# Optimization experiments

Measured on AMD Instinct MI355X. Metric: run time of the kernel, lower is better.

## Reference

```python
import jax, jax.numpy as jnp
import numpy as np

H = 128      # hidden_size
L = 2        # num_layers
IN0 = 96     # seq_feature_size + context_feature_size
OUT = 1

def _xavier(k, shape):
    fan_out, fan_in = shape
    lim = (6.0 / (fan_in + fan_out)) ** 0.5
    return jax.random.uniform(k, shape, jnp.float32, -lim, lim)

def _orth(k, n):
    q, _ = jnp.linalg.qr(jax.random.normal(k, (n, n)))
    return q.astype(jnp.float32)

def setup_inputs() -> dict:
    key = jax.random.key(0)
    ks = jax.random.split(key, 16)
    B, S, F_seq, F_ctx = 512, 512, 64, 32
    inp = {
        "seq_features": jax.random.normal(ks[0], (B, S, F_seq), jnp.float32),
        "context_features": jax.random.normal(ks[1], (B, F_ctx), jnp.float32),
    }
    for i in range(L):
        in_size = IN0 if i == 0 else H
        inp[f"tau{i}"] = jax.random.normal(ks[2 + 5 * i], (H,), jnp.float32) * 0.1
        inp[f"Win{i}"] = _xavier(ks[3 + 5 * i], (H, in_size))
        inp[f"Wrec{i}"] = _orth(ks[4 + 5 * i], H)
        inp[f"Wg{i}"] = _xavier(ks[5 + 5 * i], (H, in_size + H))
        inp[f"bg{i}"] = jnp.zeros((H,), jnp.float32)
    inp["W1"] = _xavier(ks[12], (H // 2, H))
    inp["b1"] = jnp.zeros((H // 2,), jnp.float32)
    inp["W2"] = _xavier(ks[13], (OUT, H // 2))
    inp["b2"] = jnp.zeros((OUT,), jnp.float32)
    return inp

def _cell_step(x, h, tau_p, Win, Wrec, Wg, bg):
    # LTC cell: RK4 integration of dh/dt = -h/tau + W_in x + gate * W_rec h
    tau = jax.nn.softplus(tau_p) + 1.0
    def rhs(hh):
        gate = jax.nn.sigmoid(jnp.tanh(jnp.concatenate([x, hh], axis=-1) @ Wg.T + bg))
        return -hh / tau + x @ Win.T + gate * (hh @ Wrec.T)
    k1 = rhs(h)
    k2 = rhs(h + 0.5 * k1)
    k3 = rhs(h + 0.5 * k2)
    k4 = rhs(h + k3)
    return jnp.tanh(h + (k1 + 2.0 * k2 + 2.0 * k3 + k4) / 6.0)

def reference(seq_features, context_features, tau0, Win0, Wrec0, Wg0, bg0,
              tau1, Win1, Wrec1, Wg1, bg1, W1, b1, W2, b2):
    B, S, _ = seq_features.shape
    ctx = jnp.broadcast_to(context_features[:, None, :], (B, S, context_features.shape[-1]))
    x = jnp.concatenate([seq_features, ctx], axis=-1)     # [B,S,IN0]
    xs = jnp.swapaxes(x, 0, 1)                            # [S,B,IN0] time-major
    cells = [(tau0, Win0, Wrec0, Wg0, bg0), (tau1, Win1, Wrec1, Wg1, bg1)]
    h_init = tuple(jnp.zeros((B, H), x.dtype) for _ in range(L))

    def step(hs, xt):
        new = []
        inp = xt
        for hi, p in zip(hs, cells):
            hn = _cell_step(inp, hi, *p)
            new.append(hn)
            inp = hn
        return tuple(new), None

    hs, _ = jax.lax.scan(step, h_init, xs)
    h_last = hs[-1]                                       # [B,H]
    # classifier (dropout is identity in eval mode)
    out = jax.nn.sigmoid(jax.nn.relu(h_last @ W1.T + b1) @ W2.T + b2)
    return out.reshape(B, -1)
```

## Files before the change

### kernel.cpp

```cpp
#include <hip/hip_runtime.h>


typedef _Float16 f16;
typedef _Float16 f16x4 __attribute__((ext_vector_type(4)));
typedef _Float16 f16x8 __attribute__((ext_vector_type(8)));
typedef float f32x4 __attribute__((ext_vector_type(4)));

#define NSTEP 512
#define OFF_A0 0
#define OFF_A1 32768
#define OFF_AIO 65536
#define OFF_AX 98304
#define W_TOTAL 122880

#define HQ0 0
#define HQ1 4352
#define L0A 8704
#define L0B 13056
#define L1A 17408
#define L1B 21760
#define L1H 26112
#define XT0 30464
#define XT1 32768
#define SMEM_BYTES 35072

__device__ __forceinline__ float rcp_f(float x) { return __builtin_amdgcn_rcpf(x); }
__device__ __forceinline__ float tanh_f(float x) {
  float e = __expf(2.f * x);
  return 1.f - 2.f * rcp_f(e + 1.f);
}
__device__ __forceinline__ float sig_poly(float t) {
  float s = t * t;
  float p = fmaf(s, 2.1356861e-5f, -2.1081349e-4f);
  p = fmaf(s, p, 2.0833333e-3f);
  p = fmaf(s, p, -2.0833333e-2f);
  p = fmaf(s, p, 0.25f);
  return fmaf(t, p, 0.5f);
}

#define BAR()                                            \
  do {                                                   \
    asm volatile("s_waitcnt lgkmcnt(0)" ::: "memory");   \
    __builtin_amdgcn_s_barrier();                        \
  } while (0)

__global__ __launch_bounds__(256) void prep_kernel(
    const float* __restrict__ Win0, const float* __restrict__ Wrec0,
    const float* __restrict__ Wg0, const float* __restrict__ Win1,
    const float* __restrict__ Wrec1, const float* __restrict__ Wg1,
    f16* __restrict__ W) {
  int i = blockIdx.x * 256 + threadIdx.x;
  if (i >= W_TOTAL) return;
  if (i < OFF_AX) {
    int sec = i >> 15;
    int r = i & 32767;
    int j = r & 7, lane = (r >> 3) & 63, kc = (r >> 9) & 3, sel = (r >> 11) & 1,
        w = (r >> 12) & 7;
    int row = w * 16 + (lane & 15);
    int k = kc * 32 + ((lane >> 4) << 3) + j;
    float v;
    if (sec == 0)
      v = sel ? Wrec0[row * 128 + k] : Wg0[row * 224 + 96 + k];
    else if (sec == 1)
      v = sel ? Wrec1[row * 128 + k] : Wg1[row * 256 + 128 + k];
    else
      v = sel ? Wg1[row * 256 + k] : Win1[row * 128 + k];
    W[i] = (f16)v;
  } else {
    int r = i - OFF_AX;
    int j = r & 7, lane = (r >> 3) & 63, g = r >> 9;
    int kc = g % 3, sg = g / 3;
    int sel = sg & 1, w = sg >> 1;
    int row = w * 16 + (lane & 15);
    int k = kc * 32 + ((lane >> 4) << 3) + j;
    W[i] = (f16)(sel ? Wg0[row * 224 + k] : Win0[row * 96 + k]);
  }
}

#define MFMA16(A, B, C) __builtin_amdgcn_mfma_f32_16x16x32_f16((A), (B), (C), 0, 0, 0)
#define ZERO4 ((f32x4){0.f, 0.f, 0.f, 0.f})

#define MM2(SRC)                                                    \
  {                                                                 \
    const f16* bp_ = (SRC) + c * 136 + 8 * q;                       \
    _Pragma("unroll") for (int kc_ = 0; kc_ < 4; ++kc_) {           \
      f16x8 bf_ = *(const f16x8*)(bp_ + kc_ * 32);                  \
      ga[0] = MFMA16(awg[0][kc_], bf_, ga[0]);                      \
      ra[0] = MFMA16(awr[0][kc_], bf_, ra[0]);                      \
      ga[1] = MFMA16(awg[1][kc_], bf_, ga[1]);                      \
      ra[1] = MFMA16(awr[1][kc_], bf_, ra[1]);                      \
    }                                                               \
  }

#define MMIO(SRC, KCN)                                              \
  {                                                                 \
    const f16* bp_ = (SRC) + c * 136 + 8 * q;                       \
    _Pragma("unroll") for (int kc_ = 0; kc_ < (KCN); ++kc_) {       \
      f16x8 bf_ = *(const f16x8*)(bp_ + kc_ * 32);                  \
      ga[0] = MFMA16(au[0][kc_], bf_, ga[0]);                       \
      ra[0] = MFMA16(ag2[0][kc_], bf_, ra[0]);                      \
      ga[1] = MFMA16(au[1][kc_], bf_, ga[1]);                       \
      ra[1] = MFMA16(ag2[1][kc_], bf_, ra[1]);                      \
    }                                                               \
  }

#define XPROJ(XSRC, UD, GD)                                         \
  {                                                                 \
    ZACC;                                                           \
    f16x8 bx0_ = *(const f16x8*)((XSRC) + c * 72 + 8 * q);          \
    f16x8 bx1_ = *(const f16x8*)((XSRC) + c * 72 + 32 + 8 * q);     \
    _Pragma("unroll") for (int i2_ = 0; i2_ < 2; ++i2_) {           \
      ga[i2_] = MFMA16(au[i2_][0], bx0_, ga[i2_]);                  \
      ra[i2_] = MFMA16(ag2[i2_][0], bx0_, ra[i2_]);                 \
      ga[i2_] = MFMA16(au[i2_][1], bx1_, ga[i2_]);                  \
      ra[i2_] = MFMA16(ag2[i2_][1], bx1_, ra[i2_]);                 \
      ga[i2_] = MFMA16(au[i2_][2], bctx, ga[i2_]);                  \
      ra[i2_] = MFMA16(ag2[i2_][2], bctx, ra[i2_]);                 \
      (UD)[i2_] = ga[i2_];                                          \
      _Pragma("unroll") for (int r_ = 0; r_ < 4; ++r_)              \
        (GD)[i2_][r_] = ra[i2_][r_] + bgv[i2_][r_];                 \
    }                                                               \
  }

#define GATEALL(WC, HC, DST)                                        \
  _Pragma("unroll") for (int i2_ = 0; i2_ < 2; ++i2_) {             \
    f16x4 hv_;                                                      \
    _Pragma("unroll") for (int r_ = 0; r_ < 4; ++r_) {              \
      float th_ = tanh_f(ga[i2_][r_] + gx[i2_][r_]);                \
      float gt_ = sig_poly(th_);                                    \
      float kk_ = fmaf(gt_, ra[i2_][r_],                            \
                       fmaf(-itv[i2_][r_], hhc[i2_][r_], u[i2_][r_])); \
      ksum[i2_][r_] = fmaf((WC), kk_, ksum[i2_][r_]);               \
      float hn_ = fmaf((HC), kk_, hst[i2_][r_]);                    \
      hhc[i2_][r_] = hn_;                                           \
      hv_[r_] = (f16)hn_;                                           \
    }                                                               \
    *(f16x4*)((DST) + c * 136 + jb[i2_]) = hv_;                     \
  }

#define GATEFIN(DST)                                                \
  _Pragma("unroll") for (int i2_ = 0; i2_ < 2; ++i2_) {             \
    f16x4 hv_;                                                      \
    _Pragma("unroll") for (int r_ = 0; r_ < 4; ++r_) {              \
      float th_ = tanh_f(ga[i2_][r_] + gx[i2_][r_]);                \
      float gt_ = sig_poly(th_);                                    \
      float kk_ = fmaf(gt_, ra[i2_][r_],                            \
                       fmaf(-itv[i2_][r_], hhc[i2_][r_], u[i2_][r_])); \
      float ks_ = ksum[i2_][r_] + kk_;                              \
      float hn_ = tanh_f(fmaf(ks_, 0.16666667f, hst[i2_][r_]));     \
      hst[i2_][r_] = hn_;                                           \
      hhc[i2_][r_] = hn_;                                           \
      hv_[r_] = (f16)hn_;                                           \
    }                                                               \
    *(f16x4*)((DST) + c * 136 + jb[i2_]) = hv_;                     \
  }

#define ZACC { ga[0] = ZERO4; ra[0] = ZERO4; ga[1] = ZERO4; ra[1] = ZERO4; }

__global__ __launch_bounds__(512, 1) void ltc_kernel(
    const float* __restrict__ seq, const float* __restrict__ ctx,
    const float* __restrict__ tau0p, const float* __restrict__ bg0p,
    const float* __restrict__ tau1p, const float* __restrict__ bg1p,
    const float* __restrict__ W1, const float* __restrict__ b1,
    const float* __restrict__ W2, const float* __restrict__ b2,
    const f16* __restrict__ W, float* __restrict__ out) {
  __shared__ __align__(16) char smem[SMEM_BYTES];
  f16* hq0 = (f16*)(smem + HQ0);
  f16* hq1 = (f16*)(smem + HQ1);
  f16* l0a = (f16*)(smem + L0A);
  f16* l0b = (f16*)(smem + L0B);
  f16* l1a = (f16*)(smem + L1A);
  f16* l1b = (f16*)(smem + L1B);
  f16* l1h = (f16*)(smem + L1H);
  f16* xt0 = (f16*)(smem + XT0);
  f16* xt1 = (f16*)(smem + XT1);

  const int tid = threadIdx.x;
  const int w8 = tid >> 6, lane = tid & 63;
  const int q = lane >> 4, c = lane & 15;
  const int wl = w8 & 3;
  const bool isL0 = (w8 < 4);
  const int bg = blockIdx.x;
  int jb[2];
  jb[0] = 32 * wl + 4 * q;
  jb[1] = jb[0] + 16;

  f16* bufA = isL0 ? l0a : l1a;
  f16* bufB = isL0 ? l0b : l1b;

  f16x8 awg[2][4], awr[2][4], au[2][4], ag2[2][4];
  f16x8 bctx;
  if (isL0) {
#pragma unroll
    for (int i2 = 0; i2 < 2; ++i2) {
      int T = 2 * wl + i2;
#pragma unroll
      for (int kc = 0; kc < 4; ++kc) {
        awg[i2][kc] = *(const f16x8*)(W + OFF_A0 + (((T * 2 + 0) * 4 + kc) * 64 + lane) * 8);
        awr[i2][kc] = *(const f16x8*)(W + OFF_A0 + (((T * 2 + 1) * 4 + kc) * 64 + lane) * 8);
      }
#pragma unroll
      for (int kc = 0; kc < 3; ++kc) {
        au[i2][kc] = *(const f16x8*)(W + OFF_AX + (((T * 2 + 0) * 3 + kc) * 64 + lane) * 8);
        ag2[i2][kc] = *(const f16x8*)(W + OFF_AX + (((T * 2 + 1) * 3 + kc) * 64 + lane) * 8);
      }
      au[i2][3] = (f16x8)(f16)0.f;
      ag2[i2][3] = (f16x8)(f16)0.f;
    }
    const float* cp = ctx + (bg * 16 + c) * 32 + 8 * q;
#pragma unroll
    for (int j = 0; j < 8; ++j) bctx[j] = (f16)cp[j];
  } else {
#pragma unroll
    for (int i2 = 0; i2 < 2; ++i2) {
      int T = 2 * wl + i2;
#pragma unroll
      for (int kc = 0; kc < 4; ++kc) {
        awg[i2][kc] = *(const f16x8*)(W + OFF_A1 + (((T * 2 + 0) * 4 + kc) * 64 + lane) * 8);
        awr[i2][kc] = *(const f16x8*)(W + OFF_A1 + (((T * 2 + 1) * 4 + kc) * 64 + lane) * 8);
        au[i2][kc] = *(const f16x8*)(W + OFF_AIO + (((T * 2 + 0) * 4 + kc) * 64 + lane) * 8);
        ag2[i2][kc] = *(const f16x8*)(W + OFF_AIO + (((T * 2 + 1) * 4 + kc) * 64 + lane) * 8);
      }
    }
  }

  const float* taup = isL0 ? tau0p : tau1p;
  const float* bgp = isL0 ? bg0p : bg1p;
  f32x4 itv[2], bgv[2];
#pragma unroll
  for (int i2 = 0; i2 < 2; ++i2)
#pragma unroll
    for (int r = 0; r < 4; ++r) {
      float t = taup[jb[i2] + r];
      itv[i2][r] = 1.f / (logf(1.f + __expf(t)) + 1.f);
      bgv[i2][r] = bgp[jb[i2] + r];
    }

  f32x4 hst[2], hhc[2], u[2], gx[2], ksum[2], ga[2], ra[2];
  f32x4 un[2], gxn[2];
  hst[0] = hst[1] = hhc[0] = hhc[1] = ZERO4;
  ksum[0] = ksum[1] = ZERO4;
  un[0] = un[1] = gxn[0] = gxn[1] = ZERO4;

  for (int j = tid; j < 2176; j += 512) {
    hq1[j] = (f16)0.f;
    l1h[j] = (f16)0.f;
  }
  const int bs = tid >> 4, fp = tid & 15;
  const size_t seqrow = ((size_t)(bg * 16 + bs)) * NSTEP * 64 + 4 * fp;
  float4 sq_nxt = {0.f, 0.f, 0.f, 0.f};
  float4 sq_ld = sq_nxt;
  if (tid < 256) {
    float4 sv = *(const float4*)(seq + seqrow);
    *(f16x4*)(xt0 + bs * 72 + 4 * fp) =
        (f16x4){(f16)sv.x, (f16)sv.y, (f16)sv.z, (f16)sv.w};
    sq_nxt = *(const float4*)(seq + seqrow + 64);
  }
  __syncthreads();
  if (isL0) { XPROJ(xt0, u, gx); }

#pragma unroll 1
  for (int i = 0; i <= NSTEP; ++i) {
    const f16* hprev = ((i + 1) & 1) ? hq1 : hq0;
    f16* xw = ((i + 1) & 1) ? xt1 : xt0;

    if (isL0) {
      if (i < NSTEP) {
        if (i + 2 < NSTEP)
          sq_ld = *(const float4*)(seq + seqrow + (size_t)(i + 2) * 64);
        ZACC;
        MM2(hprev);
        if (i + 1 < NSTEP)
          *(f16x4*)(xw + bs * 72 + 4 * fp) =
              (f16x4){(f16)sq_nxt.x, (f16)sq_nxt.y, (f16)sq_nxt.z, (f16)sq_nxt.w};
        ksum[0] = ZERO4; ksum[1] = ZERO4;
        GATEALL(1.0f, 0.5f, bufA);
      }
    } else {
      if (i >= 1) {
        ZACC;
        MMIO(hprev, 4);
#pragma unroll
        for (int i2 = 0; i2 < 2; ++i2) {
          u[i2] = ga[i2];
#pragma unroll
          for (int r = 0; r < 4; ++r) gx[i2][r] = ra[i2][r] + bgv[i2][r];
        }
        ZACC;
        MM2(l1h);
        ksum[0] = ZERO4; ksum[1] = ZERO4;
        GATEALL(1.0f, 0.5f, bufA);
      }
    }
    BAR();

    if (isL0) {
      if (i < NSTEP) {
        ZACC;
        MM2(bufA);
        GATEALL(2.0f, 0.5f, bufB);
        if (i + 1 < NSTEP) { XPROJ(xw, un, gxn); }
      }
    } else if (i >= 1) {
      ZACC;
      MM2(bufA);
      GATEALL(2.0f, 0.5f, bufB);
    }
    BAR();

    if ((isL0 && i < NSTEP) || (!isL0 && i >= 1)) {
      ZACC;
      MM2(bufB);
      GATEALL(2.0f, 1.0f, bufA);
    }
    BAR();

    if (isL0) {
      if (i < NSTEP) {
        ZACC;
        MM2(bufA);
        GATEFIN((i & 1) ? hq1 : hq0);
        if (i + 1 < NSTEP) {
          u[0] = un[0]; u[1] = un[1];
          gx[0] = gxn[0]; gx[1] = gxn[1];
          if (i + 2 < NSTEP) sq_nxt = sq_ld;
        }
      }
    } else if (i >= 1) {
      ZACC;
      MM2(bufA);
      GATEFIN(l1h);
    }
    BAR();
  }

  float* h1f = (float*)smem;
  if (!isL0) {
#pragma unroll
    for (int i2 = 0; i2 < 2; ++i2)
      *(f32x4*)(h1f + c * 132 + jb[i2]) = hst[i2];
  }
  __syncthreads();
  float* z1 = (float*)(smem + 16 * 132 * 4);
  {
    int b = tid >> 5, o = tid & 31;
#pragma unroll
    for (int hlf = 0; hlf < 2; ++hlf) {
      int oo = o + 32 * hlf;
      const float* wr = W1 + oo * 128;
      const float* hr = h1f + b * 132;
      float s = 0.f;
#pragma unroll
      for (int j = 0; j < 128; j += 4) {
        f32x4 wv = *(const f32x4*)(wr + j);
        f32x4 hv = *(const f32x4*)(hr + j);
        s += wv[0] * hv[0] + wv[1] * hv[1] + wv[2] * hv[2] + wv[3] * hv[3];
      }
      s += b1[oo];
      z1[b * 64 + oo] = fmaxf(s, 0.f);
    }
  }
  __syncthreads();
  if (tid < 16) {
    float s = b2[0];
#pragma unroll
    for (int o = 0; o < 64; ++o) s += z1[tid * 64 + o] * W2[o];
    out[bg * 16 + tid] = rcp_f(1.f + __expf(-s));
  }
}

extern "C" void kernel_launch(void* const* d_in, const int* in_sizes, int n_in,
                              void* d_out, int out_size, void* d_ws, size_t ws_size,
                              hipStream_t stream) {
  (void)in_sizes; (void)n_in; (void)out_size; (void)ws_size;
  const float* seq = (const float*)d_in[0];
  const float* ctx = (const float*)d_in[1];
  const float* tau0 = (const float*)d_in[2];
  const float* Win0 = (const float*)d_in[3];
  const float* Wrec0 = (const float*)d_in[4];
  const float* Wg0 = (const float*)d_in[5];
  const float* bg0 = (const float*)d_in[6];
  const float* tau1 = (const float*)d_in[7];
  const float* Win1 = (const float*)d_in[8];
  const float* Wrec1 = (const float*)d_in[9];
  const float* Wg1 = (const float*)d_in[10];
  const float* bg1 = (const float*)d_in[11];
  const float* W1 = (const float*)d_in[12];
  const float* b1 = (const float*)d_in[13];
  const float* W2 = (const float*)d_in[14];
  const float* b2 = (const float*)d_in[15];
  f16* W = (f16*)d_ws;

  prep_kernel<<<480, 256, 0, stream>>>(Win0, Wrec0, Wg0, Win1, Wrec1, Wg1, W);
  ltc_kernel<<<32, 512, 0, stream>>>(seq, ctx, tau0, bg0, tau1, bg1, W1, b1, W2,
                                     b2, W, (float*)d_out);
}
```

Before: 1.922 ms.

## Split LTC layers across producer and consumer blocks with global ring buffer

Layer 0 and layer 1 now run in separate workgroups (64 blocks total) instead of splitting one 512-thread block into two 4-wave halves. Layer 0 producer blocks push each timestep's hidden state through a 4-slot global ring, guarded by acquire/release flags, to layer 1 consumer blocks. Each wave now owns one 16-row tile instead of two, which halves per-wave MFMA and gate work on the serial critical path and uses more CUs. The cost is cross-CU spin-wait synchronisation through L2 every step, which adds latency and depends on all 64 blocks being co-resident.

```diff
diff --git a/kernel.cpp b/kernel.cpp
--- a/kernel.cpp
+++ b/kernel.cpp
@@ -5,6 +5,7 @@
 typedef _Float16 f16x4 __attribute__((ext_vector_type(4)));
 typedef _Float16 f16x8 __attribute__((ext_vector_type(8)));
 typedef float f32x4 __attribute__((ext_vector_type(4)));
+typedef unsigned long long u64;
 
 #define NSTEP 512
 #define OFF_A0 0
@@ -13,16 +14,18 @@
 #define OFF_AX 98304
 #define W_TOTAL 122880
 
+#define FLAGS_OFF 245760
+#define RING_OFF 246272
+#define RING_R 4
+#define RING_PAIR_BYTES (RING_R * 4096)
+
 #define HQ0 0
 #define HQ1 4352
-#define L0A 8704
-#define L0B 13056
-#define L1A 17408
-#define L1B 21760
-#define L1H 26112
-#define XT0 30464
-#define XT1 32768
-#define SMEM_BYTES 35072
+#define LBA 8704
+#define LBB 13056
+#define XT0 17408
+#define XT1 19712
+#define SMEM_BYTES 22272
 
 __device__ __forceinline__ float rcp_f(float x) { return __builtin_amdgcn_rcpf(x); }
 __device__ __forceinline__ float tanh_f(float x) {
@@ -49,6 +52,8 @@
     const float* __restrict__ Wg0, const float* __restrict__ Win1,
     const float* __restrict__ Wrec1, const float* __restrict__ Wg1,
     f16* __restrict__ W) {
+  if (blockIdx.x == 0 && threadIdx.x < 64)
+    ((int*)((char*)W + FLAGS_OFF))[threadIdx.x] = 0;
   int i = blockIdx.x * 256 + threadIdx.x;
   if (i >= W_TOTAL) return;
   if (i < OFF_AX) {
@@ -80,82 +85,68 @@
 #define MFMA16(A, B, C) __builtin_amdgcn_mfma_f32_16x16x32_f16((A), (B), (C), 0, 0, 0)
 #define ZERO4 ((f32x4){0.f, 0.f, 0.f, 0.f})
 
-#define MM2(SRC)                                                    \
-  {                                                                 \
+#define MM2G(SRC)                                                   \
+  {                                                                 \
+    ga = gx; ra = ZERO4;                                            \
     const f16* bp_ = (SRC) + c * 136 + 8 * q;                       \
     _Pragma("unroll") for (int kc_ = 0; kc_ < 4; ++kc_) {           \
       f16x8 bf_ = *(const f16x8*)(bp_ + kc_ * 32);                  \
-      ga[0] = MFMA16(awg[0][kc_], bf_, ga[0]);                      \
-      ra[0] = MFMA16(awr[0][kc_], bf_, ra[0]);                      \
-      ga[1] = MFMA16(awg[1][kc_], bf_, ga[1]);                      \
-      ra[1] = MFMA16(awr[1][kc_], bf_, ra[1]);                      \
+      ga = MFMA16(awg[kc_], bf_, ga);                               \
+      ra = MFMA16(awr[kc_], bf_, ra);                               \
     }                                                               \
   }
 
-#define MMIO(SRC, KCN)                                              \
-  {                                                                 \
-    const f16* bp_ = (SRC) + c * 136 + 8 * q;                       \
-    _Pragma("unroll") for (int kc_ = 0; kc_ < (KCN); ++kc_) {       \
-      f16x8 bf_ = *(const f16x8*)(bp_ + kc_ * 32);                  \
-      ga[0] = MFMA16(au[0][kc_], bf_, ga[0]);                       \
-      ra[0] = MFMA16(ag2[0][kc_], bf_, ra[0]);                      \
-      ga[1] = MFMA16(au[1][kc_], bf_, ga[1]);                       \
-      ra[1] = MFMA16(ag2[1][kc_], bf_, ra[1]);                      \
-    }                                                               \
+#define MMIO_PF()                                                   \
+  {                                                                 \
+    ga = ZERO4; ra = bgv;                                           \
+    ga = MFMA16(au[0], pf0, ga); ra = MFMA16(ag2[0], pf0, ra);      \
+    ga = MFMA16(au[1], pf1, ga); ra = MFMA16(ag2[1], pf1, ra);      \
+    ga = MFMA16(au[2], pf2, ga); ra = MFMA16(ag2[2], pf2, ra);      \
+    ga = MFMA16(au[3], pf3, ga); ra = MFMA16(ag2[3], pf3, ra);      \
+    u = ga; gx = ra;                                                \
   }
 
 #define XPROJ(XSRC, UD, GD)                                         \
   {                                                                 \
-    ZACC;                                                           \
+    f32x4 tg_ = ZERO4, tr_ = bgv;                                   \
     f16x8 bx0_ = *(const f16x8*)((XSRC) + c * 72 + 8 * q);          \
     f16x8 bx1_ = *(const f16x8*)((XSRC) + c * 72 + 32 + 8 * q);     \
-    _Pragma("unroll") for (int i2_ = 0; i2_ < 2; ++i2_) {           \
-      ga[i2_] = MFMA16(au[i2_][0], bx0_, ga[i2_]);                  \
-      ra[i2_] = MFMA16(ag2[i2_][0], bx0_, ra[i2_]);                 \
-      ga[i2_] = MFMA16(au[i2_][1], bx1_, ga[i2_]);                  \
-      ra[i2_] = MFMA16(ag2[i2_][1], bx1_, ra[i2_]);                 \
-      ga[i2_] = MFMA16(au[i2_][2], bctx, ga[i2_]);                  \
-      ra[i2_] = MFMA16(ag2[i2_][2], bctx, ra[i2_]);                 \
-      (UD)[i2_] = ga[i2_];                                          \
-      _Pragma("unroll") for (int r_ = 0; r_ < 4; ++r_)              \
-        (GD)[i2_][r_] = ra[i2_][r_] + bgv[i2_][r_];                 \
-    }                                                               \
+    tg_ = MFMA16(au[0], bx0_, tg_); tr_ = MFMA16(ag2[0], bx0_, tr_);\
+    tg_ = MFMA16(au[1], bx1_, tg_); tr_ = MFMA16(ag2[1], bx1_, tr_);\
+    tg_ = MFMA16(au[2], bctx, tg_); tr_ = MFMA16(ag2[2], bctx, tr_);\
+    (UD) = tg_; (GD) = tr_;                                         \
   }
 
 #define GATEALL(WC, HC, DST)                                        \
-  _Pragma("unroll") for (int i2_ = 0; i2_ < 2; ++i2_) {             \
+  {                                                                 \
     f16x4 hv_;                                                      \
     _Pragma("unroll") for (int r_ = 0; r_ < 4; ++r_) {              \
-      float th_ = tanh_f(ga[i2_][r_] + gx[i2_][r_]);                \
+      float th_ = tanh_f(ga[r_]);                                   \
       float gt_ = sig_poly(th_);                                    \
-      float kk_ = fmaf(gt_, ra[i2_][r_],                            \
-                       fmaf(-itv[i2_][r_], hhc[i2_][r_], u[i2_][r_])); \
-      ksum[i2_][r_] = fmaf((WC), kk_, ksum[i2_][r_]);               \
-      float hn_ = fmaf((HC), kk_, hst[i2_][r_]);                    \
-      hhc[i2_][r_] = hn_;                                           \
+      float kk_ = fmaf(gt_, ra[r_],                                 \
+                       fmaf(-itv[r_], hhc[r_], u[r_]));             \
+      ksum[r_] = fmaf((WC), kk_, ksum[r_]);                         \
+      float hn_ = fmaf((HC), kk_, hst[r_]);                         \
+      hhc[r_] = hn_;                                                \
       hv_[r_] = (f16)hn_;                                           \
     }                                                               \
-    *(f16x4*)((DST) + c * 136 + jb[i2_]) = hv_;                     \
-  }
-
-#define GATEFIN(DST)                                                \
-  _Pragma("unroll") for (int i2_ = 0; i2_ < 2; ++i2_) {             \
-    f16x4 hv_;                                                      \
-    _Pragma("unroll") for (int r_ = 0; r_ < 4; ++r_) {              \
-      float th_ = tanh_f(ga[i2_][r_] + gx[i2_][r_]);                \
-      float gt_ = sig_poly(th_);                                    \
-      float kk_ = fmaf(gt_, ra[i2_][r_],                            \
-                       fmaf(-itv[i2_][r_], hhc[i2_][r_], u[i2_][r_])); \
-      float ks_ = ksum[i2_][r_] + kk_;                              \
-      float hn_ = tanh_f(fmaf(ks_, 0.16666667f, hst[i2_][r_]));     \
-      hst[i2_][r_] = hn_;                                           \
-      hhc[i2_][r_] = hn_;                                           \
-      hv_[r_] = (f16)hn_;                                           \
-    }                                                               \
-    *(f16x4*)((DST) + c * 136 + jb[i2_]) = hv_;                     \
-  }
-
-#define ZACC { ga[0] = ZERO4; ra[0] = ZERO4; ga[1] = ZERO4; ra[1] = ZERO4; }
+    *(f16x4*)((DST) + c * 136 + jbase) = hv_;                       \
+  }
+
+#define LDPF8(KC_, DST_)                                                      \
+  {                                                                           \
+    u64* p_ = (u64*)(rs_ + c * 128 + (KC_) * 32 + 8 * q);                     \
+    u64 lo_ = __hip_atomic_load(p_, __ATOMIC_RELAXED, __HIP_MEMORY_SCOPE_AGENT); \
+    u64 hi_ = __hip_atomic_load(p_ + 1, __ATOMIC_RELAXED, __HIP_MEMORY_SCOPE_AGENT); \
+    union { u64 v[2]; f16x8 f; } uu_;                                         \
+    uu_.v[0] = lo_; uu_.v[1] = hi_;                                           \
+    DST_ = uu_.f;                                                             \
+  }
+#define LOADPF(M_)                                                  \
+  {                                                                 \
+    f16* rs_ = ring + ((M_) & (RING_R - 1)) * 2048;                 \
+    LDPF8(0, pf0); LDPF8(1, pf1); LDPF8(2, pf2); LDPF8(3, pf3);     \
+  }
 
 __global__ __launch_bounds__(512, 1) void ltc_kernel(
     const float* __restrict__ seq, const float* __restrict__ ctx,
@@ -163,183 +154,193 @@
     const float* __restrict__ tau1p, const float* __restrict__ bg1p,
     const float* __restrict__ W1, const float* __restrict__ b1,
     const float* __restrict__ W2, const float* __restrict__ b2,
-    const f16* __restrict__ W, float* __restrict__ out) {
+    const f16* __restrict__ W, char* __restrict__ ws,
+    float* __restrict__ out) {
   __shared__ __align__(16) char smem[SMEM_BYTES];
   f16* hq0 = (f16*)(smem + HQ0);
   f16* hq1 = (f16*)(smem + HQ1);
-  f16* l0a = (f16*)(smem + L0A);
-  f16* l0b = (f16*)(smem + L0B);
-  f16* l1a = (f16*)(smem + L1A);
-  f16* l1b = (f16*)(smem + L1B);
-  f16* l1h = (f16*)(smem + L1H);
+  f16* bufA = (f16*)(smem + LBA);
+  f16* bufB = (f16*)(smem + LBB);
   f16* xt0 = (f16*)(smem + XT0);
   f16* xt1 = (f16*)(smem + XT1);
 
   const int tid = threadIdx.x;
   const int w8 = tid >> 6, lane = tid & 63;
   const int q = lane >> 4, c = lane & 15;
-  const int wl = w8 & 3;
-  const bool isL0 = (w8 < 4);
-  const int bg = blockIdx.x;
-  int jb[2];
-  jb[0] = 32 * wl + 4 * q;
-  jb[1] = jb[0] + 16;
-
-  f16* bufA = isL0 ? l0a : l1a;
-  f16* bufB = isL0 ? l0b : l1b;
-
-  f16x8 awg[2][4], awr[2][4], au[2][4], ag2[2][4];
-  f16x8 bctx;
-  if (isL0) {
-#pragma unroll
-    for (int i2 = 0; i2 < 2; ++i2) {
-      int T = 2 * wl + i2;
-#pragma unroll
-      for (int kc = 0; kc < 4; ++kc) {
-        awg[i2][kc] = *(const f16x8*)(W + OFF_A0 + (((T * 2 + 0) * 4 + kc) * 64 + lane) * 8);
-        awr[i2][kc] = *(const f16x8*)(W + OFF_A0 + (((T * 2 + 1) * 4 + kc) * 64 + lane) * 8);
-      }
-#pragma unroll
-      for (int kc = 0; kc < 3; ++kc) {
-        au[i2][kc] = *(const f16x8*)(W + OFF_AX + (((T * 2 + 0) * 3 + kc) * 64 + lane) * 8);
-        ag2[i2][kc] = *(const f16x8*)(W + OFF_AX + (((T * 2 + 1) * 3 + kc) * 64 + lane) * 8);
-      }
-      au[i2][3] = (f16x8)(f16)0.f;
-      ag2[i2][3] = (f16x8)(f16)0.f;
-    }
+  const bool isProd = (blockIdx.x < 32);
+  const int bg = isProd ? blockIdx.x : blockIdx.x - 32;
+  const int jbase = 16 * w8 + 4 * q;
+
+  int* prodf = (int*)(ws + FLAGS_OFF) + bg;
+  int* consf = (int*)(ws + FLAGS_OFF + 128) + bg;
+  f16* ring = (f16*)(ws + RING_OFF + (size_t)bg * RING_PAIR_BYTES);
+
+  f16x8 awg[4], awr[4], au[4], ag2[4];
+  f16x8 bctx = (f16x8)(f16)0.f;
+  if (isProd) {
+#pragma unroll
+    for (int kc = 0; kc < 4; ++kc) {
+      awg[kc] = *(const f16x8*)(W + OFF_A0 + (((w8 * 2 + 0) * 4 + kc) * 64 + lane) * 8);
+      awr[kc] = *(const f16x8*)(W + OFF_A0 + (((w8 * 2 + 1) * 4 + kc) * 64 + lane) * 8);
+    }
+#pragma unroll
+    for (int kc = 0; kc < 3; ++kc) {
+      au[kc] = *(const f16x8*)(W + OFF_AX + (((w8 * 2 + 0) * 3 + kc) * 64 + lane) * 8);
+      ag2[kc] = *(const f16x8*)(W + OFF_AX + (((w8 * 2 + 1) * 3 + kc) * 64 + lane) * 8);
+    }
+    au[3] = (f16x8)(f16)0.f;
+    ag2[3] = (f16x8)(f16)0.f;
     const float* cp = ctx + (bg * 16 + c) * 32 + 8 * q;
 #pragma unroll
     for (int j = 0; j < 8; ++j) bctx[j] = (f16)cp[j];
   } else {
 #pragma unroll
-    for (int i2 = 0; i2 < 2; ++i2) {
-      int T = 2 * wl + i2;
-#pragma unroll
-      for (int kc = 0; kc < 4; ++kc) {
-        awg[i2][kc] = *(const f16x8*)(W + OFF_A1 + (((T * 2 + 0) * 4 + kc) * 64 + lane) * 8);
-        awr[i2][kc] = *(const f16x8*)(W + OFF_A1 + (((T * 2 + 1) * 4 + kc) * 64 + lane) * 8);
-        au[i2][kc] = *(const f16x8*)(W + OFF_AIO + (((T * 2 + 0) * 4 + kc) * 64 + lane) * 8);
-        ag2[i2][kc] = *(const f16x8*)(W + OFF_AIO + (((T * 2 + 1) * 4 + kc) * 64 + lane) * 8);
-      }
-    }
-  }
-
-  const float* taup = isL0 ? tau0p : tau1p;
-  const float* bgp = isL0 ? bg0p : bg1p;
-  f32x4 itv[2], bgv[2];
-#pragma unroll
-  for (int i2 = 0; i2 < 2; ++i2)
-#pragma unroll
-    for (int r = 0; r < 4; ++r) {
-      float t = taup[jb[i2] + r];
-      itv[i2][r] = 1.f / (logf(1.f + __expf(t)) + 1.f);
-      bgv[i2][r] = bgp[jb[i2] + r];
-    }
-
-  f32x4 hst[2], hhc[2], u[2], gx[2], ksum[2], ga[2], ra[2];
-  f32x4 un[2], gxn[2];
-  hst[0] = hst[1] = hhc[0] = hhc[1] = ZERO4;
-  ksum[0] = ksum[1] = ZERO4;
-  un[0] = un[1] = gxn[0] = gxn[1] = ZERO4;
-
-  for (int j = tid; j < 2176; j += 512) {
-    hq1[j] = (f16)0.f;
-    l1h[j] = (f16)0.f;
-  }
+    for (int kc = 0; kc < 4; ++kc) {
+      awg[kc] = *(const f16x8*)(W + OFF_A1 + (((w8 * 2 + 0) * 4 + kc) * 64 + lane) * 8);
+      awr[kc] = *(const f16x8*)(W + OFF_A1 + (((w8 * 2 + 1) * 4 + kc) * 64 + lane) * 8);
+      au[kc] = *(const f16x8*)(W + OFF_AIO + (((w8 * 2 + 0) * 4 + kc) * 64 + lane) * 8);
+      ag2[kc] = *(const f16x8*)(W + OFF_AIO + (((w8 * 2 + 1) * 4 + kc) * 64 + lane) * 8);
+    }
+  }
+
+  const float* taup = isProd ? tau0p : tau1p;
+  const float* bgp = isProd ? bg0p : bg1p;
+  f32x4 itv, bgv;
+#pragma unroll
+  for (int r = 0; r < 4; ++r) {
+    float t = taup[jbase + r];
+    itv[r] = 1.f / (logf(1.f + __expf(t)) + 1.f);
+    bgv[r] = bgp[jbase + r];
+  }
+
+  f32x4 hst = ZERO4, hhc = ZERO4, u = ZERO4, gx = ZERO4, ksum = ZERO4;
+  f32x4 ga, ra, un = ZERO4, gxn = ZERO4;
+  f16x8 pf0, pf1, pf2, pf3;
+
+  for (int j = tid; j < 2176; j += 512) hq1[j] = (f16)0.f;
+
   const int bs = tid >> 4, fp = tid & 15;
   const size_t seqrow = ((size_t)(bg * 16 + bs)) * NSTEP * 64 + 4 * fp;
   float4 sq_nxt = {0.f, 0.f, 0.f, 0.f};
   float4 sq_ld = sq_nxt;
-  if (tid < 256) {
-    float4 sv = *(const float4*)(seq + seqrow);
-    *(f16x4*)(xt0 + bs * 72 + 4 * fp) =
-        (f16x4){(f16)sv.x, (f16)sv.y, (f16)sv.z, (f16)sv.w};
-    sq_nxt = *(const float4*)(seq + seqrow + 64);
-  }
+
+  if (isProd) {
+    if (tid < 256) {
+      float4 sv = *(const float4*)(seq + seqrow);
+      *(f16x4*)(xt0 + bs * 72 + 4 * fp) =
+          (f16x4){(f16)sv.x, (f16)sv.y, (f16)sv.z, (f16)sv.w};
+      sq_nxt = *(const float4*)(seq + seqrow + 64);
+    }
+    __syncthreads();
+    XPROJ(xt0, u, gx);
+
+#pragma unroll 1
+    for (int i = 0; i < NSTEP; ++i) {
+      const f16* hprev = ((i + 1) & 1) ? hq1 : hq0;
+      f16* xw = ((i + 1) & 1) ? xt1 : xt0;
+      if (tid < 256 && i + 2 < NSTEP)
+        sq_ld = *(const float4*)(seq + seqrow + (size_t)(i + 2) * 64);
+      MM2G(hprev);
+      if (tid < 256 && i + 1 < NSTEP)
+        *(f16x4*)(xw + bs * 72 + 4 * fp) =
+            (f16x4){(f16)sq_nxt.x, (f16)sq_nxt.y, (f16)sq_nxt.z, (f16)sq_nxt.w};
+      ksum = ZERO4;
+      GATEALL(1.0f, 0.5f, bufA);
+      BAR();
+      MM2G(bufA);
+      GATEALL(2.0f, 0.5f, bufB);
+      if (i + 1 < NSTEP) { XPROJ(xw, un, gxn); }
+      BAR();
+      MM2G(bufB);
+      GATEALL(2.0f, 1.0f, bufA);
+      if (tid == 0 && i >= RING_R)
+        while (__hip_atomic_load(consf, __ATOMIC_ACQUIRE, __HIP_MEMORY_SCOPE_AGENT) <
+               i - RING_R + 1)
+          __builtin_amdgcn_s_sleep(2);
+      asm volatile("s_waitcnt vmcnt(0)" ::: "memory");
+      BAR();
+      if (tid == 0)
+        __hip_atomic_store(prodf, i, __ATOMIC_RELEASE, __HIP_MEMORY_SCOPE_AGENT);
+      MM2G(bufA);
+      {
+        f16x4 hv_;
+#pragma unroll
+        for (int r_ = 0; r_ < 4; ++r_) {
+          float th_ = tanh_f(ga[r_]);
+          float gt_ = sig_poly(th_);
+          float kk_ = fmaf(gt_, ra[r_], fmaf(-itv[r_], hhc[r_], u[r_]));
+          float ks_ = ksum[r_] + kk_;
+          float hn_ = tanh_f(fmaf(ks_, 0.16666667f, hst[r_]));
+          hst[r_] = hn_;
+          hhc[r_] = hn_;
+          hv_[r_] = (f16)hn_;
+        }
+        *(f16x4*)(((i & 1) ? hq1 : hq0) + c * 136 + jbase) = hv_;
+        u64 hb_;
+        __builtin_memcpy(&hb_, &hv_, 8);
+        __hip_atomic_store((u64*)(ring + (i & (RING_R - 1)) * 2048 + c * 128 + jbase),
+                           hb_, __ATOMIC_RELAXED, __HIP_MEMORY_SCOPE_AGENT);
+      }
+      u = un;
+      gx = gxn;
+      if (i + 2 < NSTEP) sq_nxt = sq_ld;
+      BAR();
+    }
+    asm volatile("s_waitcnt vmcnt(0)" ::: "memory");
+    __syncthreads();
+    if (tid == 0)
+      __hip_atomic_store(prodf, NSTEP, __ATOMIC_RELEASE, __HIP_MEMORY_SCOPE_AGENT);
+    return;
+  }
+
+  if (tid == 0)
+    while (__hip_atomic_load(prodf, __ATOMIC_ACQUIRE, __HIP_MEMORY_SCOPE_AGENT) < 1)
+      __builtin_amdgcn_s_sleep(2);
   __syncthreads();
-  if (isL0) { XPROJ(xt0, u, gx); }
+  LOADPF(0);
 
 #pragma unroll 1
-  for (int i = 0; i <= NSTEP; ++i) {
+  for (int i = 0; i < NSTEP; ++i) {
     const f16* hprev = ((i + 1) & 1) ? hq1 : hq0;
-    f16* xw = ((i + 1) & 1) ? xt1 : xt0;
-
-    if (isL0) {
-      if (i < NSTEP) {
-        if (i + 2 < NSTEP)
-          sq_ld = *(const float4*)(seq + seqrow + (size_t)(i + 2) * 64);
-        ZACC;
-        MM2(hprev);
-        if (i + 1 < NSTEP)
-          *(f16x4*)(xw + bs * 72 + 4 * fp) =
-              (f16x4){(f16)sq_nxt.x, (f16)sq_nxt.y, (f16)sq_nxt.z, (f16)sq_nxt.w};
-        ksum[0] = ZERO4; ksum[1] = ZERO4;
-        GATEALL(1.0f, 0.5f, bufA);
+    MMIO_PF();
+    MM2G(hprev);
+    ksum = ZERO4;
+    GATEALL(1.0f, 0.5f, bufA);
+    BAR();
+    if (tid == 0)
+      __hip_atomic_store(consf, i + 1, __ATOMIC_RELEASE, __HIP_MEMORY_SCOPE_AGENT);
+    MM2G(bufA);
+    GATEALL(2.0f, 0.5f, bufB);
+    BAR();
+    MM2G(bufB);
+    GATEALL(2.0f, 1.0f, bufA);
+    if (tid == 0 && i + 1 < NSTEP)
+      while (__hip_atomic_load(prodf, __ATOMIC_ACQUIRE, __HIP_MEMORY_SCOPE_AGENT) <
+             i + 2)
+        __builtin_amdgcn_s_sleep(2);
+    BAR();
+    MM2G(bufA);
+    {
+      f16x4 hv_;
+#pragma unroll
+      for (int r_ = 0; r_ < 4; ++r_) {
+        float th_ = tanh_f(ga[r_]);
+        float gt_ = sig_poly(th_);
+        float kk_ = fmaf(gt_, ra[r_], fmaf(-itv[r_], hhc[r_], u[r_]));
+        float ks_ = ksum[r_] + kk_;
+        float hn_ = tanh_f(fmaf(ks_, 0.16666667f, hst[r_]));
+        hst[r_] = hn_;
+        hhc[r_] = hn_;
+        hv_[r_] = (f16)hn_;
       }
-    } else {
-      if (i >= 1) {
-        ZACC;
-        MMIO(hprev, 4);
-#pragma unroll
-        for (int i2 = 0; i2 < 2; ++i2) {
-          u[i2] = ga[i2];
-#pragma unroll
-          for (int r = 0; r < 4; ++r) gx[i2][r] = ra[i2][r] + bgv[i2][r];
-        }
-        ZACC;
-        MM2(l1h);
-        ksum[0] = ZERO4; ksum[1] = ZERO4;
-        GATEALL(1.0f, 0.5f, bufA);
-      }
-    }
+      *(f16x4*)(((i & 1) ? hq1 : hq0) + c * 136 + jbase) = hv_;
+    }
+    if (i + 1 < NSTEP) { LOADPF(i + 1); }
     BAR();
-
-    if (isL0) {
-      if (i < NSTEP) {
-        ZACC;
-        MM2(bufA);
-        GATEALL(2.0f, 0.5f, bufB);
-        if (i + 1 < NSTEP) { XPROJ(xw, un, gxn); }
-      }
-    } else if (i >= 1) {
-      ZACC;
-      MM2(bufA);
-      GATEALL(2.0f, 0.5f, bufB);
-    }
-    BAR();
-
-    if ((isL0 && i < NSTEP) || (!isL0 && i >= 1)) {
-      ZACC;
-      MM2(bufB);
-      GATEALL(2.0f, 1.0f, bufA);
-    }
-    BAR();
-
-    if (isL0) {
-      if (i < NSTEP) {
-        ZACC;
-        MM2(bufA);
-        GATEFIN((i & 1) ? hq1 : hq0);
-        if (i + 1 < NSTEP) {
-          u[0] = un[0]; u[1] = un[1];
-          gx[0] = gxn[0]; gx[1] = gxn[1];
-          if (i + 2 < NSTEP) sq_nxt = sq_ld;
-        }
-      }
-    } else if (i >= 1) {
-      ZACC;
-      MM2(bufA);
-      GATEFIN(l1h);
-    }
-    BAR();
   }
 
   float* h1f = (float*)smem;
-  if (!isL0) {
-#pragma unroll
-    for (int i2 = 0; i2 < 2; ++i2)
-      *(f32x4*)(h1f + c * 132 + jb[i2]) = hst[i2];
-  }
+  *(f32x4*)(h1f + c * 132 + jbase) = hst;
   __syncthreads();
   float* z1 = (float*)(smem + 16 * 132 * 4);
   {
@@ -392,6 +393,6 @@
   f16* W = (f16*)d_ws;
 
   prep_kernel<<<480, 256, 0, stream>>>(Win0, Wrec0, Wg0, Win1, Wrec1, Wg1, W);
-  ltc_kernel<<<32, 512, 0, stream>>>(seq, ctx, tau0, bg0, tau1, bg1, W1, b1, W2,
-                                     b2, W, (float*)d_out);
-}
+  ltc_kernel<<<64, 512, 0, stream>>>(seq, ctx, tau0, bg0, tau1, bg1, W1, b1, W2,
+                                     b2, W, (char*)d_ws, (float*)d_out);
+}
```

Result: slower. 2.099 ms (+9.2%).
